# Performance work log

Hardware: AMD Instinct MI355X
Metric: run time of the kernel (lower is better)

## Reference

```python
import jax, jax.numpy as jnp
import numpy as np

KERNEL_SIZES = [1, 2, 3]
KERNEL_NUM = 11
SIGMA = 0.1
EXACT_SIGMA = 0.001
EMBED_DIM = 300
HIDDEN = 128
Q_VOCAB = 30000
D_VOCAB = 30000


def _mus_sigmas():
    mus, sigmas = [], []
    K = KERNEL_NUM
    for i in range(K):
        mu = 1.0 / (K - 1) + 2.0 * i / (K - 1) - 1.0
        sigma = SIGMA
        if mu > 1.0:
            sigma = EXACT_SIGMA
            mu = 1.0
        mus.append(mu)
        sigmas.append(sigma)
    return jnp.asarray(mus, jnp.float32), jnp.asarray(sigmas, jnp.float32)


def _conv_tanh(x_bcl, w, b, ks):
    # x_bcl: (B, C_in, L); ConstantPad1d((0, ks)) + Conv1d(kernel=ks+1) keeps length L
    y = jax.lax.conv_general_dilated(
        x_bcl, w, window_strides=(1,), padding=[(0, ks)],
        dimension_numbers=('NCW', 'OIW', 'NCW'))
    return jnp.tanh(y + b[None, :, None])  # (B, H, L)


def _l2norm(x):
    n = jnp.sqrt(jnp.sum(x * x, axis=-1, keepdims=True))
    return x / jnp.maximum(n, 1e-12)


def setup_inputs() -> dict:
    key = jax.random.key(0)
    ks = jax.random.split(key, 16)
    inp = {
        'query': jax.random.randint(ks[0], (128, 128), 0, Q_VOCAB),
        'doc': jax.random.randint(ks[1], (128, 512), 0, D_VOCAB),
        'q_emb': jax.random.normal(ks[2], (Q_VOCAB, EMBED_DIM), jnp.float32) * 0.1,
        'd_emb': jax.random.normal(ks[3], (D_VOCAB, EMBED_DIM), jnp.float32) * 0.1,
        'out_w': jax.random.normal(ks[4], (1, 3 * 3 * KERNEL_NUM), jnp.float32) * 0.1,
        'out_b': jnp.zeros((1,), jnp.float32),
    }
    for idx, k in enumerate(KERNEL_SIZES):
        fan_in = EMBED_DIM * (k + 1)
        inp[f'conv_w{idx}'] = jax.random.normal(ks[5 + 2 * idx], (HIDDEN, EMBED_DIM, k + 1), jnp.float32) / np.sqrt(fan_in)
        inp[f'conv_b{idx}'] = jnp.zeros((HIDDEN,), jnp.float32)
    return inp


def reference(query, doc, q_emb, d_emb, conv_w0, conv_b0, conv_w1, conv_b1,
              conv_w2, conv_b2, out_w, out_b):
    mus, sigmas = _mus_sigmas()
    inv2s2 = 1.0 / (2.0 * sigmas * sigmas)  # (K,)

    q_e = q_emb[query].transpose(0, 2, 1)  # (B, D, Lq)
    d_e = d_emb[doc].transpose(0, 2, 1)    # (B, D, Ld)

    cws = [(conv_w0, conv_b0), (conv_w1, conv_b1), (conv_w2, conv_b2)]
    # q_convs/d_convs share weights (same nn.Sequential appended to both lists)
    q_convs = [_l2norm(_conv_tanh(q_e, w, b, ks).transpose(0, 2, 1))
               for (w, b), ks in zip(cws, KERNEL_SIZES)]  # each (B, Lq, H)
    d_convs = [_l2norm(_conv_tanh(d_e, w, b, ks).transpose(0, 2, 1))
               for (w, b), ks in zip(cws, KERNEL_SIZES)]  # each (B, Ld, H)

    KM = []
    for qi in range(3):
        for di in range(3):
            mm = jnp.einsum('bld,brd->blr', q_convs[qi], d_convs[di])  # (B,Lq,Ld)
            # Gaussian kernel soft-histogram, vectorized over all kernels
            kern = jnp.exp(-(mm[..., None] - mus) ** 2 * inv2s2)  # (B,Lq,Ld,K)
            K = jnp.log1p(kern.sum(axis=2)).sum(axis=1)           # (B,K)
            KM.append(K)
    phi = jnp.concatenate(KM, axis=1)  # (B, 9*KERNEL_NUM)
    return phi @ out_w.T + out_b       # (B, 1)
```

## Files before the change

### kernel.cpp

```cpp
#include <hip/hip_runtime.h>
#include <hip/hip_bf16.h>

typedef __hip_bfloat16 bf16;
typedef __attribute__((ext_vector_type(8))) short short8;
typedef __attribute__((ext_vector_type(4))) float f32x4;
typedef __attribute__((ext_vector_type(2))) float f32x2;

#define NB 128
#define NH 128
#define NLQ 128
#define NLD 512
#define NEMB 300
#define XQROWS 132
#define XDROWS 516
#define XCOLS 320

__device__ __forceinline__ unsigned short bfbits(float x) {
    __hip_bfloat16 h = __float2bfloat16(x);
    return *reinterpret_cast<unsigned short*>(&h);
}

__device__ __forceinline__ float fast_tanh(float x) {
    x = fminf(9.f, fmaxf(-9.f, x));
    float e = __builtin_amdgcn_exp2f(x * 2.8853900817779268f);
    return (e - 1.f) * __builtin_amdgcn_rcpf(e + 1.f);
}

__global__ __launch_bounds__(256)
void pack_all(const int* __restrict__ q_tok, const int* __restrict__ d_tok,
              const float* __restrict__ q_emb, const float* __restrict__ d_emb,
              const float* __restrict__ cw0, const float* __restrict__ cw1,
              const float* __restrict__ cw2,
              bf16* __restrict__ Wp, bf16* __restrict__ Xq, bf16* __restrict__ Xd)
{
    int bx = blockIdx.x;
    if (bx < 1440) {
        int e = bx * 256 + threadIdx.x;
        int widx = (e >= 204800) ? 2 : (e >= 81920 ? 1 : 0);
        int off = (widx == 0) ? 0 : (widx == 1 ? 81920 : 204800);
        int el = e - off;
        int W = widx + 2;
        int ch = el >> 12;
        int cc = ch / W;
        int t  = ch - cc * W;
        int h  = (el >> 5) & 127;
        int cp = el & 31;
        int c  = cc * 32 + cp;
        const float* cw = (widx == 0) ? cw0 : (widx == 1 ? cw1 : cw2);
        float v = (c < NEMB) ? cw[(h * NEMB + c) * W + t] : 0.f;
        Wp[e] = __float2bfloat16(v);
        return;
    }
    int gid = (bx - 1440) * 256 + threadIdx.x;
    int row = gid / 20, g = gid - row * 20;
    const float* emb; bf16* dst; int tok;
    if (row < NB * XQROWS) {
        int b = row / XQROWS, l = row - b * XQROWS;
        tok = (l < NLQ) ? q_tok[b * NLQ + l] : -1;
        emb = q_emb;
        dst = Xq + (size_t)row * XCOLS + g * 16;
    } else {
        int rowd = row - NB * XQROWS;
        int b = rowd / XDROWS, l = rowd - b * XDROWS;
        tok = (l < NLD) ? d_tok[b * NLD + l] : -1;
        emb = d_emb;
        dst = Xd + (size_t)rowd * XCOLS + g * 16;
    }
    int c0 = g * 16;
    float4 v[4];
    #pragma unroll
    for (int q = 0; q < 4; ++q) {
        int c = c0 + q * 4;
        v[q] = make_float4(0.f, 0.f, 0.f, 0.f);
        if (tok >= 0 && c < NEMB)
            v[q] = *reinterpret_cast<const float4*>(emb + (size_t)tok * NEMB + c);
    }
    short8 o0, o1;
    o0[0] = (short)bfbits(v[0].x); o0[1] = (short)bfbits(v[0].y);
    o0[2] = (short)bfbits(v[0].z); o0[3] = (short)bfbits(v[0].w);
    o0[4] = (short)bfbits(v[1].x); o0[5] = (short)bfbits(v[1].y);
    o0[6] = (short)bfbits(v[1].z); o0[7] = (short)bfbits(v[1].w);
    o1[0] = (short)bfbits(v[2].x); o1[1] = (short)bfbits(v[2].y);
    o1[2] = (short)bfbits(v[2].z); o1[3] = (short)bfbits(v[2].w);
    o1[4] = (short)bfbits(v[3].x); o1[5] = (short)bfbits(v[3].y);
    o1[6] = (short)bfbits(v[3].z); o1[7] = (short)bfbits(v[3].w);
    *reinterpret_cast<short8*>(dst) = o0;
    *reinterpret_cast<short8*>(dst + 8) = o1;
}

__global__ __launch_bounds__(512, 4)
void conv_kernel(const bf16* __restrict__ Xq, const bf16* __restrict__ Xd,
                 const bf16* __restrict__ Wp,
                 const float* __restrict__ cb0, const float* __restrict__ cb1,
                 const float* __restrict__ cb2,
                 bf16* __restrict__ qn, bf16* __restrict__ dn)
{
    __shared__ bf16 Xs[2][2][132][40];
    __shared__ bf16 Bs[2][128][36];
    __shared__ float ssq[2][256];

    int bx = blockIdx.x;
    int widx = bx % 3;
    int inner = bx / 3;
    int W = widx + 2;
    const bf16* wp = Wp + ((widx == 0) ? 0 : (widx == 1 ? 81920 : 204800));
    const float* cb = (widx == 0) ? cb0 : (widx == 1 ? cb1 : cb2);

    int tid = threadIdx.x;
    int lane = tid & 63;
    int wv = tid >> 6;
    int wr = wv >> 1;
    int wc = wv & 1;
    int s_wave = wr >> 1;
    int lr_base = (wr & 1) * 64;

    bf16* outp; int L;
    int sb0, sb1, sl00, sl01;
    const bf16* xbase;
    size_t grow0, grow1;
    if (inner < 64) {
        outp = qn + (size_t)widx * NB * NLQ * NH;
        L = NLQ; sb0 = inner * 2; sb1 = sb0 + 1; sl00 = 0; sl01 = 0;
        xbase = Xq; grow0 = (size_t)sb0 * XQROWS; grow1 = (size_t)sb1 * XQROWS;
    } else {
        int i = inner - 64;
        outp = dn + (size_t)widx * NB * NLD * NH;
        L = NLD; sb0 = i >> 1; sb1 = sb0; sl00 = (i & 1) * 256; sl01 = sl00 + 128;
        xbase = Xd; grow0 = (size_t)sb0 * XDROWS + sl00; grow1 = grow0 + 128;
    }

    int sr = tid >> 2;
    int colg = tid & 3;
    const bf16* gsrc0 = xbase + (grow0 + sr) * XCOLS + colg * 8;
    const bf16* gsrc1 = xbase + (grow1 + sr) * XCOLS + colg * 8;
    bool has_tail = (tid >= 448 && tid < 480);
    int j = tid - 448;
    int ts = (j >> 2) >> 2, trr = 128 + ((j >> 2) & 3), tcolg = j & 3;
    const bf16* gsrcT = xbase + ((ts ? grow1 : grow0) + trr) * XCOLS + tcolg * 8;

    const short8* wp8 = reinterpret_cast<const short8*>(wp);
    int bh = tid >> 2, bcg = tid & 3;

    {
        short8 a0 = *reinterpret_cast<const short8*>(gsrc0);
        short8 a1 = *reinterpret_cast<const short8*>(gsrc1);
        short8 at;
        if (has_tail) at = *reinterpret_cast<const short8*>(gsrcT);
        short8 b0 = wp8[tid];
        *reinterpret_cast<short8*>(&Xs[0][0][sr][colg * 8]) = a0;
        *reinterpret_cast<short8*>(&Xs[0][1][sr][colg * 8]) = a1;
        if (has_tail) *reinterpret_cast<short8*>(&Xs[0][ts][trr][tcolg * 8]) = at;
        *reinterpret_cast<short8*>(&Bs[0][bh][bcg * 8]) = b0;
    }
    __syncthreads();

    f32x4 acc[4][4];
    #pragma unroll
    for (int m = 0; m < 4; ++m)
        #pragma unroll
        for (int n = 0; n < 4; ++n)
            acc[m][n] = (f32x4){0.f, 0.f, 0.f, 0.f};

    int nsteps = W * 10;
    int xcur = 0, bcur = 0, step = 0;
    short8 a0, a1, at;
    for (int cc = 0; cc < 10; ++cc) {
        if (cc < 9) {
            a0 = *reinterpret_cast<const short8*>(gsrc0 + (cc + 1) * 32);
            a1 = *reinterpret_cast<const short8*>(gsrc1 + (cc + 1) * 32);
            if (has_tail) at = *reinterpret_cast<const short8*>(gsrcT + (cc + 1) * 32);
        }
        for (int t = 0; t < W; ++t, ++step) {
            short8 nb;
            bool hn = (step + 1 < nsteps);
            if (hn) nb = wp8[(size_t)(step + 1) * 512 + tid];

            short8 bv[4], af[4];
            #pragma unroll
            for (int n = 0; n < 4; ++n)
                bv[n] = *reinterpret_cast<const short8*>(
                    &Bs[bcur][wc * 64 + n * 16 + (lane & 15)][(lane >> 4) * 8]);
            #pragma unroll
            for (int m = 0; m < 4; ++m)
                af[m] = *reinterpret_cast<const short8*>(
                    &Xs[xcur][s_wave][lr_base + m * 16 + (lane & 15) + t][(lane >> 4) * 8]);
            #pragma unroll
            for (int m = 0; m < 4; ++m)
                #pragma unroll
                for (int n = 0; n < 4; ++n)
                    acc[m][n] = __builtin_amdgcn_mfma_f32_16x16x32_bf16(af[m], bv[n], acc[m][n], 0, 0, 0);

            if (hn)
                *reinterpret_cast<short8*>(&Bs[bcur ^ 1][bh][bcg * 8]) = nb;
            if (t == W - 1 && cc < 9) {
                *reinterpret_cast<short8*>(&Xs[xcur ^ 1][0][sr][colg * 8]) = a0;
                *reinterpret_cast<short8*>(&Xs[xcur ^ 1][1][sr][colg * 8]) = a1;
                if (has_tail) *reinterpret_cast<short8*>(&Xs[xcur ^ 1][ts][trr][tcolg * 8]) = at;
            }
            if (hn || (t == W - 1 && cc < 9)) __syncthreads();
            bcur ^= 1;
            if (t == W - 1) xcur ^= 1;
        }
    }

    float ssl[4][4];
    #pragma unroll
    for (int m = 0; m < 4; ++m)
        #pragma unroll
        for (int i = 0; i < 4; ++i) ssl[m][i] = 0.f;

    #pragma unroll
    for (int n = 0; n < 4; ++n) {
        float bias = cb[wc * 64 + n * 16 + (lane & 15)];
        #pragma unroll
        for (int m = 0; m < 4; ++m)
            #pragma unroll
            for (int i = 0; i < 4; ++i) {
                float v = fast_tanh(acc[m][n][i] + bias);
                acc[m][n][i] = v;
                ssl[m][i] += v * v;
            }
    }
    #pragma unroll
    for (int m = 0; m < 4; ++m)
        #pragma unroll
        for (int i = 0; i < 4; ++i) {
            float s = ssl[m][i];
            s += __shfl_xor(s, 1); s += __shfl_xor(s, 2);
            s += __shfl_xor(s, 4); s += __shfl_xor(s, 8);
            ssl[m][i] = s;
        }
    if ((lane & 15) == 0) {
        #pragma unroll
        for (int m = 0; m < 4; ++m)
            #pragma unroll
            for (int i = 0; i < 4; ++i)
                ssq[wc][wr * 64 + m * 16 + (lane >> 4) * 4 + i] = ssl[m][i];
    }
    __syncthreads();
    #pragma unroll
    for (int m = 0; m < 4; ++m)
        #pragma unroll
        for (int i = 0; i < 4; ++i) {
            int r = wr * 64 + m * 16 + (lane >> 4) * 4 + i;
            float s2 = ssq[0][r] + ssq[1][r];
            float sc = 1.f / fmaxf(sqrtf(s2), 1e-12f);
            int s = r >> 7, lr = r & 127;
            int b = s ? sb1 : sb0;
            int l = (s ? sl01 : sl00) + lr;
            bf16* dst = outp + ((size_t)(b * L + l)) * NH;
            #pragma unroll
            for (int n = 0; n < 4; ++n)
                dst[wc * 64 + n * 16 + (lane & 15)] = __float2bfloat16(acc[m][n][i] * sc);
        }
}

__global__ __launch_bounds__(512, 4)
void sim_kernel(const bf16* __restrict__ qn, const bf16* __restrict__ dn,
                float* __restrict__ phi)
{
    __shared__ bf16 QDs[2][64][136];
    __shared__ float wsum[2][11];
    bf16* flat = &QDs[0][0][0];
    float (*red)[128][11] = reinterpret_cast<float(*)[128][11]>(flat);

    int blk = blockIdx.x;
    int b = blk / 9;
    int pair = blk - b * 9;
    int qi = pair / 3, di = pair - qi * 3;

    int tid = threadIdx.x, lane = tid & 63, wv = tid >> 6;
    int wr = wv >> 2;
    int wc = wv & 3;

    const bf16* qbase = qn + ((size_t)qi * NB + b) * (NLQ * NH);
    const bf16* dbase = dn + ((size_t)di * NB + b) * (NLD * NH);

    {
        int r = tid >> 2, h0 = (tid & 3) * 32;
        #pragma unroll
        for (int v = 0; v < 4; ++v)
            *reinterpret_cast<short8*>(flat + r * 136 + h0 + v * 8) =
                *reinterpret_cast<const short8*>(qbase + (size_t)r * NH + h0 + v * 8);
    }
    __syncthreads();

    short8 bq[2][4];
    #pragma unroll
    for (int n = 0; n < 2; ++n)
        #pragma unroll
        for (int kc = 0; kc < 4; ++kc)
            bq[n][kc] = *reinterpret_cast<const short8*>(
                flat + (wc * 32 + n * 16 + (lane & 15)) * 136 + kc * 32 + (lane >> 4) * 8);
    __syncthreads();

    int dr = tid >> 3, dc = (tid & 7) * 16;
    {
        short8 st0 = *reinterpret_cast<const short8*>(dbase + (size_t)dr * NH + dc);
        short8 st1 = *reinterpret_cast<const short8*>(dbase + (size_t)dr * NH + dc + 8);
        *reinterpret_cast<short8*>(&QDs[0][dr][dc]) = st0;
        *reinterpret_cast<short8*>(&QDs[0][dr][dc + 8]) = st1;
    }
    __syncthreads();

    f32x2 sums2[2][11];
    #pragma unroll
    for (int n = 0; n < 2; ++n)
        #pragma unroll
        for (int k = 0; k < 11; ++k) sums2[n][k] = (f32x2){0.f, 0.f};

    const float C1 = 1.8315638888734179e-2f;
    const float C2 = 3.3546262790251185e-4f;
    const float C3 = 6.1442123533282098e-6f;
    const float C4 = 1.1253517471925912e-7f;

    int cur = 0;
    for (int cc = 0; cc < 8; ++cc) {
        short8 st0, st1;
        if (cc < 7) {
            st0 = *reinterpret_cast<const short8*>(dbase + (size_t)((cc + 1) * 64 + dr) * NH + dc);
            st1 = *reinterpret_cast<const short8*>(dbase + (size_t)((cc + 1) * 64 + dr) * NH + dc + 8);
        }

        f32x4 acc[2][2];
        #pragma unroll
        for (int m = 0; m < 2; ++m)
            #pragma unroll
            for (int n = 0; n < 2; ++n)
                acc[m][n] = (f32x4){0.f, 0.f, 0.f, 0.f};

        #pragma unroll
        for (int kc = 0; kc < 4; ++kc) {
            short8 af[2];
            #pragma unroll
            for (int m = 0; m < 2; ++m)
                af[m] = *reinterpret_cast<const short8*>(
                    &QDs[cur][wr * 32 + m * 16 + (lane & 15)][kc * 32 + (lane >> 4) * 8]);
            #pragma unroll
            for (int m = 0; m < 2; ++m)
                #pragma unroll
                for (int n = 0; n < 2; ++n)
                    acc[m][n] = __builtin_amdgcn_mfma_f32_16x16x32_bf16(af[m], bq[n][kc], acc[m][n], 0, 0, 0);
        }

        if (cc < 7) {
            *reinterpret_cast<short8*>(&QDs[cur ^ 1][dr][dc]) = st0;
            *reinterpret_cast<short8*>(&QDs[cur ^ 1][dr][dc + 8]) = st1;
        }

        #pragma unroll
        for (int n = 0; n < 2; ++n)
            #pragma unroll
            for (int i = 0; i < 4; ++i) {
                f32x2 x2;
                x2.x = acc[0][n][i];
                x2.y = acc[1][n][i];
                f32x2 ax = x2 * 28.853900817779268f;
                f32x2 R, Ri, E4;
                R.x = __builtin_amdgcn_exp2f(ax.x);
                R.y = __builtin_amdgcn_exp2f(ax.y);
                Ri.x = __builtin_amdgcn_rcpf(R.x);
                Ri.y = __builtin_amdgcn_rcpf(R.y);
                f32x2 d4 = x2 + 0.1f;
                f32x2 t = d4 * d4 * (-72.134752044448169f);
                E4.x = __builtin_amdgcn_exp2f(t.x);
                E4.y = __builtin_amdgcn_exp2f(t.y);
                sums2[n][4] += E4;
                f32x2 u = E4 * R;
                sums2[n][5] += u;
                u *= R; u *= C1; sums2[n][6] += u;
                u *= R; u *= C2; sums2[n][7] += u;
                u *= R; u *= C3; sums2[n][8] += u;
                u *= R; u *= C4; sums2[n][9] += u;
                f32x2 w = E4 * Ri; w *= C1; sums2[n][3] += w;
                w *= Ri; w *= C2; sums2[n][2] += w;
                w *= Ri; w *= C3; sums2[n][1] += w;
                w *= Ri; w *= C4; sums2[n][0] += w;
                if (__any(fmaxf(x2.x, x2.y) > 0.98f)) {
                    f32x2 d1 = x2 - 1.0f;
                    f32x2 t1 = d1 * d1 * (-721347.52044448f);
                    f32x2 e;
                    e.x = __builtin_amdgcn_exp2f(t1.x);
                    e.y = __builtin_amdgcn_exp2f(t1.y);
                    sums2[n][10] += e;
                }
            }

        __syncthreads();
        cur ^= 1;
    }

    #pragma unroll
    for (int n = 0; n < 2; ++n)
        #pragma unroll
        for (int k = 0; k < 11; ++k) {
            float s = sums2[n][k].x + sums2[n][k].y;
            s += __shfl_xor(s, 16);
            s += __shfl_xor(s, 32);
            sums2[n][k].x = s;
        }
    if ((lane >> 4) == 0) {
        #pragma unroll
        for (int n = 0; n < 2; ++n)
            #pragma unroll
            for (int k = 0; k < 11; ++k)
                red[wr][wc * 32 + n * 16 + (lane & 15)][k] = sums2[n][k].x;
    }
    __syncthreads();
    if (tid < 128) {
        float lv[11];
        #pragma unroll
        for (int k = 0; k < 11; ++k)
            lv[k] = log1pf(red[0][tid][k] + red[1][tid][k]);
        #pragma unroll
        for (int k = 0; k < 11; ++k) {
            float s = lv[k];
            s += __shfl_xor(s, 1); s += __shfl_xor(s, 2); s += __shfl_xor(s, 4);
            s += __shfl_xor(s, 8); s += __shfl_xor(s, 16); s += __shfl_xor(s, 32);
            lv[k] = s;
        }
        if ((tid & 63) == 0) {
            #pragma unroll
            for (int k = 0; k < 11; ++k) wsum[tid >> 6][k] = lv[k];
        }
    }
    __syncthreads();
    if (tid < 11) phi[b * 99 + pair * 11 + tid] = wsum[0][tid] + wsum[1][tid];
}

__global__ void final_kernel(const float* __restrict__ phi, const float* __restrict__ ow,
                             const float* __restrict__ obias, float* __restrict__ out)
{
    int b = threadIdx.x;
    float s = obias[0];
    #pragma unroll
    for (int j = 0; j < 99; ++j) s += phi[b * 99 + j] * ow[j];
    out[b] = s;
}

extern "C" void kernel_launch(void* const* d_in, const int* in_sizes, int n_in,
                              void* d_out, int out_size, void* d_ws, size_t ws_size,
                              hipStream_t stream)
{
    const int*   query = (const int*)d_in[0];
    const int*   doc   = (const int*)d_in[1];
    const float* q_emb = (const float*)d_in[2];
    const float* d_emb = (const float*)d_in[3];
    const float* out_w = (const float*)d_in[4];
    const float* out_b = (const float*)d_in[5];
    const float* cw0 = (const float*)d_in[6];
    const float* cb0 = (const float*)d_in[7];
    const float* cw1 = (const float*)d_in[8];
    const float* cb1 = (const float*)d_in[9];
    const float* cw2 = (const float*)d_in[10];
    const float* cb2 = (const float*)d_in[11];

    const size_t QN = (size_t)NB * NLQ * NH;
    const size_t DN = (size_t)NB * NLD * NH;
    const size_t XQN = (size_t)NB * XQROWS * XCOLS;
    const size_t XDN = (size_t)NB * XDROWS * XCOLS;

    bf16* Wp = (bf16*)d_ws;
    bf16* Xq = Wp + 368640;
    bf16* Xd = Xq + XQN;
    bf16* qn = Xd + XDN;
    bf16* dn = qn + 3 * QN;
    float* phi = (float*)(dn + 3 * DN);

    pack_all<<<7920, 256, 0, stream>>>(query, doc, q_emb, d_emb, cw0, cw1, cw2, Wp, Xq, Xd);
    conv_kernel<<<960, 512, 0, stream>>>(Xq, Xd, Wp, cb0, cb1, cb2, qn, dn);
    sim_kernel<<<NB * 9, 512, 0, stream>>>(qn, dn, phi);
    final_kernel<<<1, 128, 0, stream>>>(phi, out_w, out_b, (float*)d_out);
}
```

Baseline: 208.3 us.

## Split sim kernel over query halves and defer Gaussian constants to final scale

The similarity kernel grid doubles: each block now handles 64 query rows instead of 128, halving per-thread accumulators and MFMA tiles. Per-block partial log-sums go to a partial buffer that the final kernel combines. The per-element multiplications by C1..C4 in the Gaussian recurrence are removed, and the accumulated products are rescaled once per query row before log1p. This trades less work per element and lower register pressure for reloading each doc matrix twice. Dropping the scale constants risks overflow or underflow in the unscaled sums.

```diff
diff --git a/kernel.cpp b/kernel.cpp
--- a/kernel.cpp
+++ b/kernel.cpp
@@ -257,41 +257,40 @@
 
 __global__ __launch_bounds__(512, 4)
 void sim_kernel(const bf16* __restrict__ qn, const bf16* __restrict__ dn,
-                float* __restrict__ phi)
+                float* __restrict__ phi_part)
 {
     __shared__ bf16 QDs[2][64][136];
-    __shared__ float wsum[2][11];
     bf16* flat = &QDs[0][0][0];
-    float (*red)[128][11] = reinterpret_cast<float(*)[128][11]>(flat);
+    float (*red)[64][11] = reinterpret_cast<float(*)[64][11]>(flat);
 
     int blk = blockIdx.x;
-    int b = blk / 9;
-    int pair = blk - b * 9;
+    int b = blk / 18;
+    int rem = blk - b * 18;
+    int pair = rem >> 1;
+    int half = rem & 1;
     int qi = pair / 3, di = pair - qi * 3;
 
     int tid = threadIdx.x, lane = tid & 63, wv = tid >> 6;
     int wr = wv >> 2;
     int wc = wv & 3;
 
-    const bf16* qbase = qn + ((size_t)qi * NB + b) * (NLQ * NH);
+    const bf16* qbase = qn + ((size_t)qi * NB + b) * (NLQ * NH) + (size_t)half * 64 * NH;
     const bf16* dbase = dn + ((size_t)di * NB + b) * (NLD * NH);
 
     {
-        int r = tid >> 2, h0 = (tid & 3) * 32;
-        #pragma unroll
-        for (int v = 0; v < 4; ++v)
-            *reinterpret_cast<short8*>(flat + r * 136 + h0 + v * 8) =
-                *reinterpret_cast<const short8*>(qbase + (size_t)r * NH + h0 + v * 8);
-    }
-    __syncthreads();
-
-    short8 bq[2][4];
-    #pragma unroll
-    for (int n = 0; n < 2; ++n)
-        #pragma unroll
-        for (int kc = 0; kc < 4; ++kc)
-            bq[n][kc] = *reinterpret_cast<const short8*>(
-                flat + (wc * 32 + n * 16 + (lane & 15)) * 136 + kc * 32 + (lane >> 4) * 8);
+        int r = tid >> 3, h0 = (tid & 7) * 16;
+        *reinterpret_cast<short8*>(flat + r * 136 + h0) =
+            *reinterpret_cast<const short8*>(qbase + (size_t)r * NH + h0);
+        *reinterpret_cast<short8*>(flat + r * 136 + h0 + 8) =
+            *reinterpret_cast<const short8*>(qbase + (size_t)r * NH + h0 + 8);
+    }
+    __syncthreads();
+
+    short8 bq[4];
+    #pragma unroll
+    for (int kc = 0; kc < 4; ++kc)
+        bq[kc] = *reinterpret_cast<const short8*>(
+            flat + (wc * 16 + (lane & 15)) * 136 + kc * 32 + (lane >> 4) * 8);
     __syncthreads();
 
     int dr = tid >> 3, dc = (tid & 7) * 16;
@@ -303,16 +302,9 @@
     }
     __syncthreads();
 
-    f32x2 sums2[2][11];
-    #pragma unroll
-    for (int n = 0; n < 2; ++n)
-        #pragma unroll
-        for (int k = 0; k < 11; ++k) sums2[n][k] = (f32x2){0.f, 0.f};
-
-    const float C1 = 1.8315638888734179e-2f;
-    const float C2 = 3.3546262790251185e-4f;
-    const float C3 = 6.1442123533282098e-6f;
-    const float C4 = 1.1253517471925912e-7f;
+    f32x2 sums2[11];
+    #pragma unroll
+    for (int k = 0; k < 11; ++k) sums2[k] = (f32x2){0.f, 0.f};
 
     int cur = 0;
     for (int cc = 0; cc < 8; ++cc) {
@@ -322,12 +314,9 @@
             st1 = *reinterpret_cast<const short8*>(dbase + (size_t)((cc + 1) * 64 + dr) * NH + dc + 8);
         }
 
-        f32x4 acc[2][2];
-        #pragma unroll
-        for (int m = 0; m < 2; ++m)
-            #pragma unroll
-            for (int n = 0; n < 2; ++n)
-                acc[m][n] = (f32x4){0.f, 0.f, 0.f, 0.f};
+        f32x4 acc[2];
+        acc[0] = (f32x4){0.f, 0.f, 0.f, 0.f};
+        acc[1] = (f32x4){0.f, 0.f, 0.f, 0.f};
 
         #pragma unroll
         for (int kc = 0; kc < 4; ++kc) {
@@ -338,9 +327,7 @@
                     &QDs[cur][wr * 32 + m * 16 + (lane & 15)][kc * 32 + (lane >> 4) * 8]);
             #pragma unroll
             for (int m = 0; m < 2; ++m)
-                #pragma unroll
-                for (int n = 0; n < 2; ++n)
-                    acc[m][n] = __builtin_amdgcn_mfma_f32_16x16x32_bf16(af[m], bq[n][kc], acc[m][n], 0, 0, 0);
+                acc[m] = __builtin_amdgcn_mfma_f32_16x16x32_bf16(af[m], bq[kc], acc[m], 0, 0, 0);
         }
 
         if (cc < 7) {
@@ -349,69 +336,76 @@
         }
 
         #pragma unroll
-        for (int n = 0; n < 2; ++n)
-            #pragma unroll
-            for (int i = 0; i < 4; ++i) {
-                f32x2 x2;
-                x2.x = acc[0][n][i];
-                x2.y = acc[1][n][i];
-                f32x2 ax = x2 * 28.853900817779268f;
-                f32x2 R, Ri, E4;
-                R.x = __builtin_amdgcn_exp2f(ax.x);
-                R.y = __builtin_amdgcn_exp2f(ax.y);
-                Ri.x = __builtin_amdgcn_rcpf(R.x);
-                Ri.y = __builtin_amdgcn_rcpf(R.y);
-                f32x2 d4 = x2 + 0.1f;
-                f32x2 t = d4 * d4 * (-72.134752044448169f);
-                E4.x = __builtin_amdgcn_exp2f(t.x);
-                E4.y = __builtin_amdgcn_exp2f(t.y);
-                sums2[n][4] += E4;
-                f32x2 u = E4 * R;
-                sums2[n][5] += u;
-                u *= R; u *= C1; sums2[n][6] += u;
-                u *= R; u *= C2; sums2[n][7] += u;
-                u *= R; u *= C3; sums2[n][8] += u;
-                u *= R; u *= C4; sums2[n][9] += u;
-                f32x2 w = E4 * Ri; w *= C1; sums2[n][3] += w;
-                w *= Ri; w *= C2; sums2[n][2] += w;
-                w *= Ri; w *= C3; sums2[n][1] += w;
-                w *= Ri; w *= C4; sums2[n][0] += w;
-                if (__any(fmaxf(x2.x, x2.y) > 0.98f)) {
-                    f32x2 d1 = x2 - 1.0f;
-                    f32x2 t1 = d1 * d1 * (-721347.52044448f);
-                    f32x2 e;
-                    e.x = __builtin_amdgcn_exp2f(t1.x);
-                    e.y = __builtin_amdgcn_exp2f(t1.y);
-                    sums2[n][10] += e;
-                }
+        for (int i = 0; i < 4; ++i) {
+            f32x2 x2;
+            x2.x = acc[0][i];
+            x2.y = acc[1][i];
+            f32x2 ax = x2 * 28.853900817779268f;
+            f32x2 R, Ri, E4;
+            R.x = __builtin_amdgcn_exp2f(ax.x);
+            R.y = __builtin_amdgcn_exp2f(ax.y);
+            Ri.x = __builtin_amdgcn_rcpf(R.x);
+            Ri.y = __builtin_amdgcn_rcpf(R.y);
+            f32x2 d4 = x2 + 0.1f;
+            f32x2 t = d4 * d4 * (-72.134752044448169f);
+            E4.x = __builtin_amdgcn_exp2f(t.x);
+            E4.y = __builtin_amdgcn_exp2f(t.y);
+            sums2[4] += E4;
+            f32x2 u = E4 * R;
+            sums2[5] += u;
+            u *= R; sums2[6] += u;
+            u *= R; sums2[7] += u;
+            u *= R; sums2[8] += u;
+            u *= R; sums2[9] += u;
+            f32x2 w = E4 * Ri;
+            sums2[3] += w;
+            w *= Ri; sums2[2] += w;
+            w *= Ri; sums2[1] += w;
+            w *= Ri; sums2[0] += w;
+            if (__any(fmaxf(x2.x, x2.y) > 0.98f)) {
+                f32x2 d1 = x2 - 1.0f;
+                f32x2 t1 = d1 * d1 * (-721347.52044448f);
+                f32x2 e;
+                e.x = __builtin_amdgcn_exp2f(t1.x);
+                e.y = __builtin_amdgcn_exp2f(t1.y);
+                sums2[10] += e;
             }
+        }
 
         __syncthreads();
         cur ^= 1;
     }
 
     #pragma unroll
-    for (int n = 0; n < 2; ++n)
-        #pragma unroll
-        for (int k = 0; k < 11; ++k) {
-            float s = sums2[n][k].x + sums2[n][k].y;
-            s += __shfl_xor(s, 16);
-            s += __shfl_xor(s, 32);
-            sums2[n][k].x = s;
-        }
+    for (int k = 0; k < 11; ++k) {
+        float s = sums2[k].x + sums2[k].y;
+        s += __shfl_xor(s, 16);
+        s += __shfl_xor(s, 32);
+        sums2[k].x = s;
+    }
     if ((lane >> 4) == 0) {
         #pragma unroll
-        for (int n = 0; n < 2; ++n)
-            #pragma unroll
-            for (int k = 0; k < 11; ++k)
-                red[wr][wc * 32 + n * 16 + (lane & 15)][k] = sums2[n][k].x;
-    }
-    __syncthreads();
-    if (tid < 128) {
+        for (int k = 0; k < 11; ++k)
+            red[wr][wc * 16 + (lane & 15)][k] = sums2[k].x;
+    }
+    __syncthreads();
+
+    if (tid < 64) {
+        const float scale[11] = {
+            4.2483542552915889e-18f,
+            3.7751345442790977e-11f,
+            6.1442123533282098e-6f,
+            1.8315638888734179e-2f,
+            1.f, 1.f,
+            1.8315638888734179e-2f,
+            6.1442123533282098e-6f,
+            3.7751345442790977e-11f,
+            4.2483542552915889e-18f,
+            1.f };
         float lv[11];
         #pragma unroll
         for (int k = 0; k < 11; ++k)
-            lv[k] = log1pf(red[0][tid][k] + red[1][tid][k]);
+            lv[k] = log1pf(scale[k] * (red[0][tid][k] + red[1][tid][k]));
         #pragma unroll
         for (int k = 0; k < 11; ++k) {
             float s = lv[k];
@@ -419,22 +413,27 @@
             s += __shfl_xor(s, 8); s += __shfl_xor(s, 16); s += __shfl_xor(s, 32);
             lv[k] = s;
         }
-        if ((tid & 63) == 0) {
-            #pragma unroll
-            for (int k = 0; k < 11; ++k) wsum[tid >> 6][k] = lv[k];
-        }
-    }
-    __syncthreads();
-    if (tid < 11) phi[b * 99 + pair * 11 + tid] = wsum[0][tid] + wsum[1][tid];
-}
-
-__global__ void final_kernel(const float* __restrict__ phi, const float* __restrict__ ow,
+        if (tid == 0) {
+            #pragma unroll
+            for (int k = 0; k < 11; ++k)
+                phi_part[(size_t)blk * 11 + k] = lv[k];
+        }
+    }
+}
+
+__global__ void final_kernel(const float* __restrict__ phi_part,
+                             const float* __restrict__ ow,
                              const float* __restrict__ obias, float* __restrict__ out)
 {
     int b = threadIdx.x;
     float s = obias[0];
     #pragma unroll
-    for (int j = 0; j < 99; ++j) s += phi[b * 99 + j] * ow[j];
+    for (int pair = 0; pair < 9; ++pair)
+        #pragma unroll
+        for (int k = 0; k < 11; ++k) {
+            size_t base = ((size_t)b * 18 + pair * 2) * 11 + k;
+            s += (phi_part[base] + phi_part[base + 11]) * ow[pair * 11 + k];
+        }
     out[b] = s;
 }
 
@@ -465,10 +464,10 @@
     bf16* Xd = Xq + XQN;
     bf16* qn = Xd + XDN;
     bf16* dn = qn + 3 * QN;
-    float* phi = (float*)(dn + 3 * DN);
+    float* phi_part = (float*)(dn + 3 * DN);
 
     pack_all<<<7920, 256, 0, stream>>>(query, doc, q_emb, d_emb, cw0, cw1, cw2, Wp, Xq, Xd);
     conv_kernel<<<960, 512, 0, stream>>>(Xq, Xd, Wp, cb0, cb1, cb2, qn, dn);
-    sim_kernel<<<NB * 9, 512, 0, stream>>>(qn, dn, phi);
-    final_kernel<<<1, 128, 0, stream>>>(phi, out_w, out_b, (float*)d_out);
-}
+    sim_kernel<<<NB * 9 * 2, 512, 0, stream>>>(qn, dn, phi_part);
+    final_kernel<<<1, 128, 0, stream>>>(phi_part, out_w, out_b, (float*)d_out);
+}
```

After: 210.9 us. About the same (+1.3%).
